# Kernel tuning notes

Hardware: AMD Instinct MI355X
Metric: run time of the kernel (lower is better)

The kernel has to match this reference:

```python
import jax, jax.numpy as jnp
import numpy as np
import math

NUM_HEADS = 8

def setup_inputs() -> dict:
    key = jax.random.key(0)
    k1, k2, k3 = jax.random.split(key, 3)
    B, N, C = 16, 4096, 512
    x = jax.random.normal(k1, (B, N, C), dtype=jnp.float32)
    qkv_w = jax.random.normal(k2, (3 * C, C), dtype=jnp.float32) * 0.02
    proj_w = jax.random.normal(k3, (C, C), dtype=jnp.float32) * 0.02
    proj_b = jnp.zeros((C,), dtype=jnp.float32)
    return {"x": x, "qkv_w": qkv_w, "proj_w": proj_w, "proj_b": proj_b}


def reference(x, qkv_w, proj_w, proj_b):
    # Attention with is_mask=1: row-wise windowed attention.
    B, N, C = x.shape
    H = W = int(math.isqrt(N))
    nh = NUM_HEADS
    hd = C // nh
    scale = hd ** (-0.5)

    # fold rows into batch: (B*H, W, C)
    img = x.reshape(B * H, W, C)
    # qkv linear (no bias): (B*H, W, 3C) -> (3, B*H, nh, W, hd)
    qkv = jnp.einsum('bwc,dc->bwd', img, qkv_w)
    qkv = qkv.reshape(B * H, W, 3, nh, hd).transpose(2, 0, 3, 1, 4)
    q, k, v = qkv[0], qkv[1], qkv[2]

    # scaled dot-product attention within each row window
    attn = jnp.einsum('bhqd,bhkd->bhqk', q, k) * scale
    attn = jax.nn.softmax(attn, axis=-1)
    out = jnp.einsum('bhqk,bhkd->bhqd', attn, v)   # (B*H, nh, W, hd)
    out = out.transpose(0, 2, 1, 3).reshape(B, N, C)

    # output projection
    return jnp.einsum('bnc,dc->bnd', out, proj_w) + proj_b
```

## Files before the change

### kernel.cpp

```cpp
#include <hip/hip_runtime.h>
#include <cstdint>
#include <cstddef>

typedef _Float16 half8 __attribute__((ext_vector_type(8)));
typedef _Float16 half4 __attribute__((ext_vector_type(4)));
typedef float f32x4 __attribute__((ext_vector_type(4)));

#define GLDS16(g, l) __builtin_amdgcn_global_load_lds( \
    (__attribute__((address_space(1))) void*)(g), \
    (__attribute__((address_space(3))) void*)(l), 16, 0, 0)

__global__ __launch_bounds__(256) void cvt_f32_f16(const float* __restrict__ src,
                                                   _Float16* __restrict__ dst, int n) {
  int i = (blockIdx.x * 256 + threadIdx.x) * 8;
  if (i >= n) return;
  float4 a = *(const float4*)(src + i);
  float4 b = *(const float4*)(src + i + 4);
  half8 h;
  h[0] = (_Float16)a.x; h[1] = (_Float16)a.y; h[2] = (_Float16)a.z; h[3] = (_Float16)a.w;
  h[4] = (_Float16)b.x; h[5] = (_Float16)b.y; h[6] = (_Float16)b.z; h[7] = (_Float16)b.w;
  *(half8*)(dst + i) = h;
}

template<int NOUT, int NT, bool BIAS>
__global__ __launch_bounds__(256, 3) void gemm_bt(const _Float16* __restrict__ A,
                                                  const _Float16* __restrict__ Bw,
                                                  const float* __restrict__ bias,
                                                  void* __restrict__ Cout) {
  constexpr int K = 512;
  __shared__ union {
    struct { _Float16 As[4096]; _Float16 Bs[4096]; } s;
    float E[2][16][132];
  } u;
  const int id  = blockIdx.x;
  const int xcd = id & 7;
  const int jj  = id >> 3;
  const int by  = (jj / NT) * 8 + xcd;
  const int bx  = jj % NT;
  const int m_base = by * 128, n_base = bx * 128;

  const int t    = threadIdx.x;
  const int lane = t & 63;
  const int wid  = t >> 6;
  const int wm   = wid >> 1, wn = wid & 1;
  const int cl   = lane & 15, q = lane >> 4;

  f32x4 acc[4][4] = {};

  const int s0 = t, s1 = t + 256;
  const int r0 = ((s0 >> 6) << 4) | (s0 & 15), c0 = (s0 >> 4) & 3;
  const int r1 = ((s1 >> 6) << 4) | (s1 & 15), c1 = (s1 >> 4) & 3;
  const _Float16* a0 = A  + (size_t)(m_base + r0) * K + c0 * 8;
  const _Float16* a1 = A  + (size_t)(m_base + r1) * K + c1 * 8;
  const _Float16* b0 = Bw + (size_t)(n_base + r0) * K + c0 * 8;
  const _Float16* b1 = Bw + (size_t)(n_base + r1) * K + c1 * 8;
  char* adst0 = (char*)u.s.As + s0 * 16;
  char* adst1 = (char*)u.s.As + s1 * 16;
  char* bdst0 = (char*)u.s.Bs + s0 * 16;
  char* bdst1 = (char*)u.s.Bs + s1 * 16;

  const int lane8 = lane * 8;

  for (int k0 = 0; k0 < K; k0 += 32) {
    GLDS16(a0 + k0, adst0);
    GLDS16(a1 + k0, adst1);
    GLDS16(b0 + k0, bdst0);
    GLDS16(b1 + k0, bdst1);
    __syncthreads();
    half8 af[4], bf[4];
#pragma unroll
    for (int i = 0; i < 4; i++) af[i] = *(const half8*)(u.s.As + (wm * 4 + i) * 512 + lane8);
#pragma unroll
    for (int i = 0; i < 4; i++) bf[i] = *(const half8*)(u.s.Bs + (wn * 4 + i) * 512 + lane8);
#pragma unroll
    for (int mt = 0; mt < 4; mt++)
#pragma unroll
      for (int nt = 0; nt < 4; nt++)
        acc[mt][nt] = __builtin_amdgcn_mfma_f32_16x16x32_f16(af[mt], bf[nt], acc[mt][nt], 0, 0, 0);
    __syncthreads();
  }

  const int ebnd = t >> 7, erow = (t >> 3) & 15, ecs = t & 7;
#pragma unroll
  for (int mt = 0; mt < 4; mt++) {
#pragma unroll
    for (int nt = 0; nt < 4; nt++)
#pragma unroll
      for (int r = 0; r < 4; r++)
        u.E[wm][q * 4 + r][wn * 64 + nt * 16 + cl] = acc[mt][nt][r];
    __syncthreads();
    const size_t rg = (size_t)(m_base + ebnd * 64 + mt * 16 + erow);
#pragma unroll
    for (int j = 0; j < 4; j++) {
      const int ch = ((ecs - erow) & 7) + 8 * j;
      const int cc = ch * 4;
      float4 e = *(const float4*)&u.E[ebnd][erow][cc];
      if constexpr (BIAS) {
        const float4 bb = *(const float4*)(bias + n_base + cc);
        e.x += bb.x; e.y += bb.y; e.z += bb.z; e.w += bb.w;
        *(float4*)((float*)Cout + rg * NOUT + n_base + cc) = e;
      } else {
        half4 hv;
        hv[0] = (_Float16)e.x; hv[1] = (_Float16)e.y;
        hv[2] = (_Float16)e.z; hv[3] = (_Float16)e.w;
        *(half4*)((_Float16*)Cout + rg * NOUT + n_base + cc) = hv;
      }
    }
    __syncthreads();
  }
}

__global__ __launch_bounds__(256, 3) void attn_win(const _Float16* __restrict__ QKV,
                                                   _Float16* __restrict__ Out) {
  __shared__ _Float16 Qs[4096];
  __shared__ _Float16 Ks[4096];
  __shared__ _Float16 Vt[64][72];
  __shared__ _Float16 Ps[64][72];
  __shared__ _Float16 Os[64][72];
  const int h = blockIdx.x, b = blockIdx.y;
  const int t = threadIdx.x;
  const int lane = t & 63, wid = t >> 6;
  const int cl = lane & 15, q = lane >> 4;

  {
    const int s0 = t, s1 = t + 256;
    const int r0 = ((s0 >> 7) << 4) | (s0 & 15), ch0 = (s0 >> 4) & 7;
    const int r1 = ((s1 >> 7) << 4) | (s1 & 15), ch1 = (s1 >> 4) & 7;
    const _Float16* g0 = QKV + (size_t)(b * 64 + r0) * 1536 + h * 64 + ch0 * 8;
    const _Float16* g1 = QKV + (size_t)(b * 64 + r1) * 1536 + h * 64 + ch1 * 8;
    GLDS16(g0,       (char*)Qs + s0 * 16);
    GLDS16(g1,       (char*)Qs + s1 * 16);
    GLDS16(g0 + 512, (char*)Ks + s0 * 16);
    GLDS16(g1 + 512, (char*)Ks + s1 * 16);

    const int vj = t & 63, vp = t >> 6;
    const _Float16* vsrc = QKV + (size_t)(b * 64 + vj) * 1536 + 1024 + h * 64 + vp * 16;
    half8 v0 = *(const half8*)vsrc;
    half8 v1 = *(const half8*)(vsrc + 8);
#pragma unroll
    for (int i = 0; i < 8; i++) Vt[vp * 16 + i][vj] = v0[i];
#pragma unroll
    for (int i = 0; i < 8; i++) Vt[vp * 16 + 8 + i][vj] = v1[i];
  }
  __syncthreads();

  const int m0 = wid * 16;
  const int lane8 = lane * 8;

  f32x4 s[4] = {};
#pragma unroll
  for (int ks = 0; ks < 2; ks++) {
    half8 a = *(const half8*)(Qs + wid * 1024 + ks * 512 + lane8);
#pragma unroll
    for (int nt = 0; nt < 4; nt++) {
      half8 bb = *(const half8*)(Ks + nt * 1024 + ks * 512 + lane8);
      s[nt] = __builtin_amdgcn_mfma_f32_16x16x32_f16(a, bb, s[nt], 0, 0, 0);
    }
  }

  constexpr float SC = 0.125f * 1.44269504088896340736f;
#pragma unroll
  for (int r = 0; r < 4; r++) {
    float mx = fmaxf(fmaxf(s[0][r], s[1][r]), fmaxf(s[2][r], s[3][r]));
    mx = fmaxf(mx, __shfl_xor(mx, 1));
    mx = fmaxf(mx, __shfl_xor(mx, 2));
    mx = fmaxf(mx, __shfl_xor(mx, 4));
    mx = fmaxf(mx, __shfl_xor(mx, 8));
    float e[4], ssum = 0.f;
#pragma unroll
    for (int nt = 0; nt < 4; nt++) { e[nt] = exp2f((s[nt][r] - mx) * SC); ssum += e[nt]; }
    ssum += __shfl_xor(ssum, 1);
    ssum += __shfl_xor(ssum, 2);
    ssum += __shfl_xor(ssum, 4);
    ssum += __shfl_xor(ssum, 8);
    float inv = 1.f / ssum;
    const int row = m0 + q * 4 + r;
#pragma unroll
    for (int nt = 0; nt < 4; nt++) Ps[row][nt * 16 + cl] = (_Float16)(e[nt] * inv);
  }
  __syncthreads();

  f32x4 o[4] = {};
#pragma unroll
  for (int ks = 0; ks < 2; ks++) {
    half8 a = *(const half8*)&Ps[m0 + cl][ks * 32 + q * 8];
#pragma unroll
    for (int nt = 0; nt < 4; nt++) {
      half8 bb = *(const half8*)&Vt[nt * 16 + cl][ks * 32 + q * 8];
      o[nt] = __builtin_amdgcn_mfma_f32_16x16x32_f16(a, bb, o[nt], 0, 0, 0);
    }
  }
#pragma unroll
  for (int nt = 0; nt < 4; nt++)
#pragma unroll
    for (int r = 0; r < 4; r++)
      Os[m0 + q * 4 + r][nt * 16 + cl] = (_Float16)o[nt][r];
  __syncthreads();

  {
    const int row = t >> 2, cs = t & 3;
    half8 h0 = *(const half8*)&Os[row][cs * 16];
    half8 h1 = *(const half8*)&Os[row][cs * 16 + 8];
    _Float16* dst = Out + (size_t)(b * 64 + row) * 512 + h * 64 + cs * 16;
    *(half8*)dst = h0;
    *((half8*)dst + 1) = h1;
  }
}

extern "C" void kernel_launch(void* const* d_in, const int* in_sizes, int n_in,
                              void* d_out, int out_size, void* d_ws, size_t ws_size,
                              hipStream_t stream) {
  const float* x      = (const float*)d_in[0];
  const float* qkv_w  = (const float*)d_in[1];
  const float* proj_w = (const float*)d_in[2];
  const float* proj_b = (const float*)d_in[3];
  float* out = (float*)d_out;

  char* ws = (char*)d_ws;
  _Float16* QKVh = (_Float16*)ws;
  _Float16* Xh   = (_Float16*)(ws + 201326592);
  _Float16* Outh = Xh;
  _Float16* Wq   = (_Float16*)(ws + 268435456);
  _Float16* Wp   = (_Float16*)(ws + 270008320);

  cvt_f32_f16<<<16384, 256, 0, stream>>>(x, Xh, 16 * 4096 * 512);
  cvt_f32_f16<<<384, 256, 0, stream>>>(qkv_w, Wq, 1536 * 512);
  cvt_f32_f16<<<128, 256, 0, stream>>>(proj_w, Wp, 512 * 512);
  gemm_bt<1536, 12, false><<<6144, 256, 0, stream>>>(Xh, Wq, nullptr, QKVh);
  attn_win<<<dim3(8, 1024), 256, 0, stream>>>(QKVh, Outh);
  gemm_bt<512, 4, true><<<2048, 256, 0, stream>>>(Outh, Wp, proj_b, out);
}
```

Before: 580.6 us.

## Double GEMM K-step to 64 and use per-wave LDS buffers in attention

The GEMM now loads a 64-wide K slice per iteration, with a doubled LDS footprint, so it needs half as many barrier pairs per tile. The attention kernel gives each wave its own P and O LDS region, with P stored in the MFMA operand layout. Block-wide __syncthreads between softmax, PV and the output store are replaced by per-wave lgkmcnt waits. Costs are larger GEMM LDS, which may cut occupancy below the launch-bounds target, and reliance on wave-local ordering for correctness.

Result: slower. 593.7 us (+2.3%).

```diff
diff --git a/kernel.cpp b/kernel.cpp
--- a/kernel.cpp
+++ b/kernel.cpp
@@ -29,7 +29,7 @@
                                                   void* __restrict__ Cout) {
   constexpr int K = 512;
   __shared__ union {
-    struct { _Float16 As[4096]; _Float16 Bs[4096]; } s;
+    struct { _Float16 As[8192]; _Float16 Bs[8192]; } s;
     float E[2][16][132];
   } u;
   const int id  = blockIdx.x;
@@ -47,36 +47,42 @@
 
   f32x4 acc[4][4] = {};
 
-  const int s0 = t, s1 = t + 256;
-  const int r0 = ((s0 >> 6) << 4) | (s0 & 15), c0 = (s0 >> 4) & 3;
-  const int r1 = ((s1 >> 6) << 4) | (s1 & 15), c1 = (s1 >> 4) & 3;
-  const _Float16* a0 = A  + (size_t)(m_base + r0) * K + c0 * 8;
-  const _Float16* a1 = A  + (size_t)(m_base + r1) * K + c1 * 8;
-  const _Float16* b0 = Bw + (size_t)(n_base + r0) * K + c0 * 8;
-  const _Float16* b1 = Bw + (size_t)(n_base + r1) * K + c1 * 8;
-  char* adst0 = (char*)u.s.As + s0 * 16;
-  char* adst1 = (char*)u.s.As + s1 * 16;
-  char* bdst0 = (char*)u.s.Bs + s0 * 16;
-  char* bdst1 = (char*)u.s.Bs + s1 * 16;
+  const _Float16* aS[4]; const _Float16* bS[4];
+  char* aD[4]; char* bD[4];
+#pragma unroll
+  for (int j = 0; j < 4; j++) {
+    const int s = t + j * 256;
+    const int r = ((s >> 7) << 4) | (s & 15);
+    const int c = (s >> 4) & 7;
+    aS[j] = A  + (size_t)(m_base + r) * K + c * 8;
+    bS[j] = Bw + (size_t)(n_base + r) * K + c * 8;
+    aD[j] = (char*)u.s.As + s * 16;
+    bD[j] = (char*)u.s.Bs + s * 16;
+  }
 
   const int lane8 = lane * 8;
 
-  for (int k0 = 0; k0 < K; k0 += 32) {
-    GLDS16(a0 + k0, adst0);
-    GLDS16(a1 + k0, adst1);
-    GLDS16(b0 + k0, bdst0);
-    GLDS16(b1 + k0, bdst1);
-    __syncthreads();
-    half8 af[4], bf[4];
-#pragma unroll
-    for (int i = 0; i < 4; i++) af[i] = *(const half8*)(u.s.As + (wm * 4 + i) * 512 + lane8);
-#pragma unroll
-    for (int i = 0; i < 4; i++) bf[i] = *(const half8*)(u.s.Bs + (wn * 4 + i) * 512 + lane8);
-#pragma unroll
-    for (int mt = 0; mt < 4; mt++)
-#pragma unroll
-      for (int nt = 0; nt < 4; nt++)
-        acc[mt][nt] = __builtin_amdgcn_mfma_f32_16x16x32_f16(af[mt], bf[nt], acc[mt][nt], 0, 0, 0);
+  for (int k0 = 0; k0 < K; k0 += 64) {
+#pragma unroll
+    for (int j = 0; j < 4; j++) GLDS16(aS[j] + k0, aD[j]);
+#pragma unroll
+    for (int j = 0; j < 4; j++) GLDS16(bS[j] + k0, bD[j]);
+    __syncthreads();
+#pragma unroll
+    for (int kk = 0; kk < 2; kk++) {
+      half8 af[4], bf[4];
+#pragma unroll
+      for (int i = 0; i < 4; i++)
+        af[i] = *(const half8*)(u.s.As + (wm * 4 + i) * 1024 + kk * 512 + lane8);
+#pragma unroll
+      for (int i = 0; i < 4; i++)
+        bf[i] = *(const half8*)(u.s.Bs + (wn * 4 + i) * 1024 + kk * 512 + lane8);
+#pragma unroll
+      for (int mt = 0; mt < 4; mt++)
+#pragma unroll
+        for (int nt = 0; nt < 4; nt++)
+          acc[mt][nt] = __builtin_amdgcn_mfma_f32_16x16x32_f16(af[mt], bf[nt], acc[mt][nt], 0, 0, 0);
+    }
     __syncthreads();
   }
 
@@ -115,8 +121,8 @@
   __shared__ _Float16 Qs[4096];
   __shared__ _Float16 Ks[4096];
   __shared__ _Float16 Vt[64][72];
-  __shared__ _Float16 Ps[64][72];
-  __shared__ _Float16 Os[64][72];
+  __shared__ _Float16 Ps[4][1024];
+  __shared__ _Float16 Os[4][1024];
   const int h = blockIdx.x, b = blockIdx.y;
   const int t = threadIdx.x;
   const int lane = t & 63, wid = t >> 6;
@@ -144,7 +150,6 @@
   }
   __syncthreads();
 
-  const int m0 = wid * 16;
   const int lane8 = lane * 8;
 
   f32x4 s[4] = {};
@@ -174,19 +179,21 @@
     ssum += __shfl_xor(ssum, 4);
     ssum += __shfl_xor(ssum, 8);
     float inv = 1.f / ssum;
-    const int row = m0 + q * 4 + r;
-#pragma unroll
-    for (int nt = 0; nt < 4; nt++) Ps[row][nt * 16 + cl] = (_Float16)(e[nt] * inv);
-  }
-  __syncthreads();
+#pragma unroll
+    for (int nt = 0; nt < 4; nt++) {
+      const int idx = ((nt * 2 + (cl >> 3)) * 16 + q * 4 + r) * 8 + (cl & 7);
+      Ps[wid][idx] = (_Float16)(e[nt] * inv);
+    }
+  }
+  asm volatile("s_waitcnt lgkmcnt(0)" ::: "memory");
 
   f32x4 o[4] = {};
 #pragma unroll
-  for (int ks = 0; ks < 2; ks++) {
-    half8 a = *(const half8*)&Ps[m0 + cl][ks * 32 + q * 8];
+  for (int kk = 0; kk < 2; kk++) {
+    half8 a = *(const half8*)(Ps[wid] + kk * 512 + lane8);
 #pragma unroll
     for (int nt = 0; nt < 4; nt++) {
-      half8 bb = *(const half8*)&Vt[nt * 16 + cl][ks * 32 + q * 8];
+      half8 bb = *(const half8*)&Vt[nt * 16 + cl][kk * 32 + q * 8];
       o[nt] = __builtin_amdgcn_mfma_f32_16x16x32_f16(a, bb, o[nt], 0, 0, 0);
     }
   }
@@ -194,14 +201,15 @@
   for (int nt = 0; nt < 4; nt++)
 #pragma unroll
     for (int r = 0; r < 4; r++)
-      Os[m0 + q * 4 + r][nt * 16 + cl] = (_Float16)o[nt][r];
-  __syncthreads();
+      Os[wid][(q * 4 + r) * 64 + nt * 16 + cl] = (_Float16)o[nt][r];
+  asm volatile("s_waitcnt lgkmcnt(0)" ::: "memory");
 
   {
-    const int row = t >> 2, cs = t & 3;
-    half8 h0 = *(const half8*)&Os[row][cs * 16];
-    half8 h1 = *(const half8*)&Os[row][cs * 16 + 8];
-    _Float16* dst = Out + (size_t)(b * 64 + row) * 512 + h * 64 + cs * 16;
+    const int row = lane >> 2, cs = lane & 3;
+    const _Float16* sp = Os[wid] + row * 64 + cs * 16;
+    half8 h0 = *(const half8*)sp;
+    half8 h1 = *(const half8*)(sp + 8);
+    _Float16* dst = Out + (size_t)(b * 64 + wid * 16 + row) * 512 + h * 64 + cs * 16;
     *(half8*)dst = h0;
     *((half8*)dst + 1) = h1;
   }
```
